# Kernel tuning notes

Measured on AMD Instinct MI355X. Metric: run time of the kernel, lower is better.

## Reference

```python
import jax, jax.numpy as jnp
import numpy as np
from jax import lax

N = 4096
INPUT_SIZE = 2048
HIDDEN = 256
HEADS = 4
T_POWER = 6
K_KNN = 30   # N >= 300 branch in compute_markov_tensor_optic
KA = 10      # int(k/3)


def setup_inputs() -> dict:
    key = jax.random.key(0)
    k1, k2, k3, k4, k5 = jax.random.split(key, 5)
    bound = 1.0 / np.sqrt(INPUT_SIZE)
    return {
        "input_tensor": jax.random.normal(k1, (N, INPUT_SIZE), dtype=jnp.float32),
        "Wq": jax.random.uniform(k2, (HEADS, HIDDEN, INPUT_SIZE), jnp.float32, -bound, bound),
        "bq": jax.random.uniform(k3, (HEADS, HIDDEN), jnp.float32, -bound, bound),
        "Wk": jax.random.uniform(k4, (HEADS, HIDDEN, INPUT_SIZE), jnp.float32, -bound, bound),
        "bk": jax.random.uniform(k5, (HEADS, HIDDEN), jnp.float32, -bound, bound),
    }


def _markov(q, k):
    # q, k: [N, HIDDEN]; pairwise Euclidean distances via gram trick
    sq = (jnp.sum(q * q, axis=1)[:, None]
          + jnp.sum(k * k, axis=1)[None, :]
          - 2.0 * (q @ k.T))
    d = jnp.sqrt(jnp.maximum(sq, 0.0) + 1e-10)          # [N, N]
    # adaptive bandwidth: (KA)-th smallest distance per row
    md = jnp.sort(d, axis=1)[:, KA]                      # [N]
    d = d / (md[:, None] + 1e-10)
    aff = jnp.exp(-(d ** 2))                             # epsilon = 1
    # knn pruning: keep entries >= k-th largest per row
    kth = lax.top_k(aff, K_KNN)[0][:, -1]                # [N]
    aff = aff * (aff >= kth[:, None]).astype(aff.dtype)
    idx = jnp.arange(aff.shape[0])
    aff = aff.at[idx, idx].set(1.0)
    return aff + aff.T


def reference(input_tensor, Wq, bq, Wk, bk):
    # per-head projections: [HEADS, N, HIDDEN]
    q = jnp.einsum('nd,hkd->hnk', input_tensor, Wq) + bq[:, None, :]
    k = jnp.einsum('nd,hkd->hnk', input_tensor, Wk) + bk[:, None, :]
    aff = jax.vmap(_markov)(q, k)                        # [HEADS, N, N]
    probs = jax.nn.softmax(aff, axis=-1)
    probs_t = jnp.linalg.matrix_power(probs, T_POWER)    # batched matrix power
    ctx = jnp.einsum('hnm,md->hnd', probs_t, input_tensor)  # [HEADS, N, INPUT_SIZE]
    return jnp.mean(ctx, axis=0)
```

## Files before the change

### kernel.cpp

```cpp
#include <hip/hip_runtime.h>
#include <hip/hip_bf16.h>
#include <math.h>

#define NN 4096
#define DIN 2048
#define HID 256
#define NHEADS 4
#define CAP 1024
#define OVF_CAP 131072
#define PW 128

__global__ __launch_bounds__(256) void proj_kernel(
    const float* __restrict__ X, const float* __restrict__ Wq, const float* __restrict__ bq,
    const float* __restrict__ Wk, const float* __restrict__ bk,
    float* __restrict__ qbuf, float* __restrict__ kbuf, int h)
{
    const int isK = blockIdx.z;
    const float* W    = (isK ? Wk : Wq) + (size_t)h * HID * DIN;
    const float* bias = (isK ? bk : bq) + h * HID;
    float* out = isK ? kbuf : qbuf;

    const int bm = blockIdx.x * 64;
    const int bn = blockIdx.y * 64;
    const int t  = threadIdx.x;
    const int tx = t & 15, ty = t >> 4;
    const int lr = t >> 2, lk = (t & 3) * 4;

    __shared__ float As[16][68];
    __shared__ float Bs[16][68];
    float acc[4][4] = {};

    for (int k0 = 0; k0 < DIN; k0 += 16) {
        float4 av = *(const float4*)(X + (size_t)(bm + lr) * DIN + k0 + lk);
        float4 bv = *(const float4*)(W + (size_t)(bn + lr) * DIN + k0 + lk);
        As[lk+0][lr]=av.x; As[lk+1][lr]=av.y; As[lk+2][lr]=av.z; As[lk+3][lr]=av.w;
        Bs[lk+0][lr]=bv.x; Bs[lk+1][lr]=bv.y; Bs[lk+2][lr]=bv.z; Bs[lk+3][lr]=bv.w;
        __syncthreads();
        #pragma unroll
        for (int kk = 0; kk < 16; ++kk) {
            const float4 a4 = *(const float4*)&As[kk][ty*4];
            const float4 b4 = *(const float4*)&Bs[kk][tx*4];
            const float a[4] = {a4.x,a4.y,a4.z,a4.w};
            const float b[4] = {b4.x,b4.y,b4.z,b4.w};
            #pragma unroll
            for (int i = 0; i < 4; ++i)
                #pragma unroll
                for (int j = 0; j < 4; ++j)
                    acc[i][j] = fmaf(a[i], b[j], acc[i][j]);
        }
        __syncthreads();
    }
    #pragma unroll
    for (int i = 0; i < 4; ++i) {
        const int m = bm + ty*4 + i;
        float4 o;
        o.x = acc[i][0] + bias[bn+tx*4+0];
        o.y = acc[i][1] + bias[bn+tx*4+1];
        o.z = acc[i][2] + bias[bn+tx*4+2];
        o.w = acc[i][3] + bias[bn+tx*4+3];
        *(float4*)(out + (size_t)m * HID + bn + tx*4) = o;
    }
}

__global__ __launch_bounds__(64) void rownorm_kernel(
    const float* __restrict__ q, const float* __restrict__ k,
    float* __restrict__ sqq, float* __restrict__ sqk)
{
    const int row = blockIdx.x;
    const int lane = threadIdx.x;
    const float* src = (blockIdx.y ? k : q) + (size_t)row * HID;
    float4 v = *(const float4*)(src + lane * 4);
    float s = v.x*v.x + v.y*v.y + v.z*v.z + v.w*v.w;
    for (int off = 32; off; off >>= 1) s += __shfl_down(s, off);
    if (lane == 0) (blockIdx.y ? sqk : sqq)[row] = s;
}

__global__ __launch_bounds__(256) void dist_kernel(
    const float* __restrict__ q, const float* __restrict__ k,
    const float* __restrict__ sqq, const float* __restrict__ sqk,
    float* __restrict__ Dm)
{
    const int bm = blockIdx.x * 64;
    const int bn = blockIdx.y * 64;
    const int t  = threadIdx.x;
    const int tx = t & 15, ty = t >> 4;
    const int lr = t >> 2, lk = (t & 3) * 4;

    __shared__ float As[16][68];
    __shared__ float Bs[16][68];
    float acc[4][4] = {};

    for (int k0 = 0; k0 < HID; k0 += 16) {
        float4 av = *(const float4*)(q + (size_t)(bm + lr) * HID + k0 + lk);
        float4 bv = *(const float4*)(k + (size_t)(bn + lr) * HID + k0 + lk);
        As[lk+0][lr]=av.x; As[lk+1][lr]=av.y; As[lk+2][lr]=av.z; As[lk+3][lr]=av.w;
        Bs[lk+0][lr]=bv.x; Bs[lk+1][lr]=bv.y; Bs[lk+2][lr]=bv.z; Bs[lk+3][lr]=bv.w;
        __syncthreads();
        #pragma unroll
        for (int kk = 0; kk < 16; ++kk) {
            const float4 a4 = *(const float4*)&As[kk][ty*4];
            const float4 b4 = *(const float4*)&Bs[kk][tx*4];
            const float a[4] = {a4.x,a4.y,a4.z,a4.w};
            const float b[4] = {b4.x,b4.y,b4.z,b4.w};
            #pragma unroll
            for (int i = 0; i < 4; ++i)
                #pragma unroll
                for (int j = 0; j < 4; ++j)
                    acc[i][j] = fmaf(a[i], b[j], acc[i][j]);
        }
        __syncthreads();
    }
    #pragma unroll
    for (int i = 0; i < 4; ++i) {
        const int m = bm + ty*4 + i;
        const float sm = sqq[m];
        float4 o;
        float v0 = sm + sqk[bn+tx*4+0] - 2.0f*acc[i][0];
        float v1 = sm + sqk[bn+tx*4+1] - 2.0f*acc[i][1];
        float v2 = sm + sqk[bn+tx*4+2] - 2.0f*acc[i][2];
        float v3 = sm + sqk[bn+tx*4+3] - 2.0f*acc[i][3];
        o.x = sqrtf(fmaxf(v0, 0.0f) + 1e-10f);
        o.y = sqrtf(fmaxf(v1, 0.0f) + 1e-10f);
        o.z = sqrtf(fmaxf(v2, 0.0f) + 1e-10f);
        o.w = sqrtf(fmaxf(v3, 0.0f) + 1e-10f);
        *(float4*)(Dm + (size_t)m * NN + bn + tx*4) = o;
    }
}

__device__ unsigned radix_kth_smallest(const unsigned* s, int lane, int K)
{
    unsigned lo = 0u, hi = 0xFFFFFFFFu;
    while (lo < hi) {
        unsigned mid = lo + ((hi - lo) >> 1);
        int c = 0;
        #pragma unroll 8
        for (int i = 0; i < 64; ++i) c += (s[i*64 + lane] <= mid) ? 1 : 0;
        for (int off = 32; off; off >>= 1) c += __shfl_xor(c, off);
        if (c >= K) hi = mid; else lo = mid + 1;
    }
    return lo;
}

__global__ __launch_bounds__(64) void select_kernel(
    const float* __restrict__ Dm, float* __restrict__ mdp, float* __restrict__ kth)
{
    __shared__ unsigned s[NN];
    const int row = blockIdx.x;
    const int lane = threadIdx.x;
    const float* src = Dm + (size_t)row * NN;
    for (int c = 0; c < 16; ++c) {
        const int base = c*256 + lane*4;
        float4 v = *(const float4*)(src + base);
        s[base+0] = __float_as_uint(v.x);
        s[base+1] = __float_as_uint(v.y);
        s[base+2] = __float_as_uint(v.z);
        s[base+3] = __float_as_uint(v.w);
    }
    __syncthreads();
    unsigned v11 = radix_kth_smallest(s, lane, 11);
    unsigned v30 = radix_kth_smallest(s, lane, 30);
    if (lane == 0) {
        float md = __uint_as_float(v11) + 1e-10f;
        float t  = __uint_as_float(v30) / md;
        mdp[row] = md;
        kth[row] = expf(-(t*t));
    }
}

__global__ __launch_bounds__(256) void aff_kernel(
    float* __restrict__ Dm, const float* __restrict__ mdp, const float* __restrict__ kthv)
{
    const size_t idx4 = ((size_t)blockIdx.x * 256 + threadIdx.x) * 4;
    const int i = (int)(idx4 >> 12);
    const int j = (int)(idx4 & 4095);
    const float m = mdp[i];
    const float kt = kthv[i];
    float4 v = *(float4*)(Dm + idx4);
    float t0 = v.x / m, t1 = v.y / m, t2 = v.z / m, t3 = v.w / m;
    float a0 = expf(-(t0*t0)), a1 = expf(-(t1*t1)), a2 = expf(-(t2*t2)), a3 = expf(-(t3*t3));
    a0 = (a0 >= kt) ? a0 : 0.0f;
    a1 = (a1 >= kt) ? a1 : 0.0f;
    a2 = (a2 >= kt) ? a2 : 0.0f;
    a3 = (a3 >= kt) ? a3 : 0.0f;
    if (j+0 == i) a0 = 1.0f;
    if (j+1 == i) a1 = 1.0f;
    if (j+2 == i) a2 = 1.0f;
    if (j+3 == i) a3 = 1.0f;
    v.x = a0; v.y = a1; v.z = a2; v.w = a3;
    *(float4*)(Dm + idx4) = v;
}

__global__ __launch_bounds__(256) void sym_kernel(float* __restrict__ Dm)
{
    int rem = blockIdx.x;
    int bi = 0;
    while (rem >= 64 - bi) { rem -= 64 - bi; ++bi; }
    const int bj = bi + rem;

    __shared__ float T1[64][65];
    __shared__ float T2[64][65];
    const int t = threadIdx.x;
    const int lr = t >> 4;
    const int lc4 = (t & 15) * 4;

    #pragma unroll
    for (int rr = 0; rr < 4; ++rr) {
        const int r = rr*16 + lr;
        float4 v1 = *(const float4*)(Dm + (size_t)(bi*64 + r) * NN + bj*64 + lc4);
        T1[r][lc4+0]=v1.x; T1[r][lc4+1]=v1.y; T1[r][lc4+2]=v1.z; T1[r][lc4+3]=v1.w;
        float4 v2 = *(const float4*)(Dm + (size_t)(bj*64 + r) * NN + bi*64 + lc4);
        T2[r][lc4+0]=v2.x; T2[r][lc4+1]=v2.y; T2[r][lc4+2]=v2.z; T2[r][lc4+3]=v2.w;
    }
    __syncthreads();
    #pragma unroll
    for (int rr = 0; rr < 4; ++rr) {
        const int r = rr*16 + lr;
        float4 o1;
        o1.x = T1[r][lc4+0] + T2[lc4+0][r];
        o1.y = T1[r][lc4+1] + T2[lc4+1][r];
        o1.z = T1[r][lc4+2] + T2[lc4+2][r];
        o1.w = T1[r][lc4+3] + T2[lc4+3][r];
        *(float4*)(Dm + (size_t)(bi*64 + r) * NN + bj*64 + lc4) = o1;
        if (bi != bj) {
            float4 o2;
            o2.x = T2[r][lc4+0] + T1[lc4+0][r];
            o2.y = T2[r][lc4+1] + T1[lc4+1][r];
            o2.z = T2[r][lc4+2] + T1[lc4+2][r];
            o2.w = T2[r][lc4+3] + T1[lc4+3][r];
            *(float4*)(Dm + (size_t)(bj*64 + r) * NN + bi*64 + lc4) = o2;
        }
    }
}

__global__ __launch_bounds__(64) void zero_ovf_kernel(int* __restrict__ ovf_cnt)
{
    if (threadIdx.x == 0) *ovf_cnt = 0;
}

__global__ __launch_bounds__(256) void stats_extract_kernel(
    const float* __restrict__ A, float* __restrict__ cvec, int* __restrict__ nnz,
    int* __restrict__ cols, float* __restrict__ vals,
    int* __restrict__ ovf_cnt, int* __restrict__ ovf_row,
    int* __restrict__ ovf_col, float* __restrict__ ovf_val)
{
    __shared__ float srow[NN];
    __shared__ float red[8];
    __shared__ int cnt;
    const int row = blockIdx.x, t = threadIdx.x;
    const int lane = t & 63, wid = t >> 6;
    const float* src = A + (size_t)row * NN;

    float mx = -1e30f;
    #pragma unroll
    for (int c = 0; c < 4; ++c) {
        const int base = c*1024 + t*4;
        float4 v = *(const float4*)(src + base);
        *(float4*)&srow[base] = v;
        mx = fmaxf(mx, fmaxf(fmaxf(v.x, v.y), fmaxf(v.z, v.w)));
    }
    for (int off = 32; off; off >>= 1) mx = fmaxf(mx, __shfl_xor(mx, off));
    if (lane == 0) red[wid] = mx;
    __syncthreads();
    mx = fmaxf(fmaxf(red[0], red[1]), fmaxf(red[2], red[3]));

    float sum = 0.0f;
    #pragma unroll
    for (int c = 0; c < 4; ++c) {
        const int base = c*1024 + t*4;
        float4 v = *(float4*)&srow[base];
        sum += expf(v.x-mx) + expf(v.y-mx) + expf(v.z-mx) + expf(v.w-mx);
    }
    for (int off = 32; off; off >>= 1) sum += __shfl_xor(sum, off);
    if (lane == 0) red[4 + wid] = sum;
    if (t == 0) cnt = 0;
    __syncthreads();
    sum = red[4] + red[5] + red[6] + red[7];
    const float ci = expf(-mx) / sum;
    if (t == 0) cvec[row] = ci;

    for (int c = 0; c < 16; ++c) {
        const int j = c*256 + t;
        const float a = srow[j];
        if (a != 0.0f) {
            const float v = expf(a - mx)/sum - ci;
            int p = atomicAdd(&cnt, 1);
            if (p < CAP) {
                cols[(size_t)row*CAP + p] = j;
                vals[(size_t)row*CAP + p] = v;
            } else {
                int q = atomicAdd(ovf_cnt, 1);
                if (q < OVF_CAP) {
                    ovf_row[q] = row;
                    ovf_col[q] = j;
                    ovf_val[q] = v;
                }
            }
        }
    }
    __syncthreads();
    if (t == 0) {
        const int c2 = min(cnt, CAP);
        const int e2 = min((c2 + 7) & ~7, CAP);
        for (int p = c2; p < e2; ++p) {
            cols[(size_t)row*CAP + p] = 0;
            vals[(size_t)row*CAP + p] = 0.0f;
        }
        nnz[row] = e2 == c2 ? c2 : e2;
    }
}

__global__ __launch_bounds__(256) void colsum_partial_kernel(
    const float* __restrict__ Y, float* __restrict__ part)
{
    const int cc = blockIdx.y * 256 + threadIdx.x;
    const int r0 = blockIdx.x * 128;
    float s = 0.0f;
    for (int r = 0; r < 128; ++r) s += Y[(size_t)(r0 + r) * DIN + cc];
    part[(size_t)blockIdx.x * DIN + cc] = s;
}

__global__ __launch_bounds__(256) void colsum_final_kernel(
    const float* __restrict__ part, float* __restrict__ colsum)
{
    const int cc = blockIdx.x * 256 + threadIdx.x;
    float s = 0.0f;
    #pragma unroll
    for (int r = 0; r < 32; ++r) s += part[(size_t)r * DIN + cc];
    colsum[cc] = s;
}

__global__ __launch_bounds__(256) void spmm_kernel(
    const float* __restrict__ Y, const float* __restrict__ colsum,
    const float* __restrict__ cvec, const int* __restrict__ nnz,
    const int* __restrict__ cols, const float* __restrict__ vals,
    float* __restrict__ Yout, int mode)
{
    const int wave = threadIdx.x >> 6, lane = threadIdx.x & 63;
    const int row = __builtin_amdgcn_readfirstlane(blockIdx.x * 4 + wave);
    const int c = blockIdx.y * PW + lane * 2;

    const int n = nnz[row];
    const float ci = cvec[row];
    const int*   rc = cols + (size_t)row * CAP;
    const float* rv = vals + (size_t)row * CAP;

    const float2 s = *(const float2*)(colsum + c);
    float ax = ci * s.x, ay = ci * s.y;

    for (int base = 0; base < n; base += 8) {
        float2 y[8];
        #pragma unroll
        for (int u = 0; u < 8; ++u) {
            const int j = rc[base + u];
            y[u] = *(const float2*)(Y + (size_t)j * DIN + c);
        }
        #pragma unroll
        for (int u = 0; u < 8; ++u) {
            const float v = rv[base + u];
            ax = fmaf(v, y[u].x, ax);
            ay = fmaf(v, y[u].y, ay);
        }
    }

    float* dst = Yout + (size_t)row * DIN + c;
    float2 o;
    if (mode == 0)      { o.x = ax;       o.y = ay; }
    else if (mode == 1) { o.x = 0.25f*ax; o.y = 0.25f*ay; }
    else {
        const float2 p = *(const float2*)dst;
        o.x = p.x + 0.25f*ax; o.y = p.y + 0.25f*ay;
    }
    *(float2*)dst = o;
}

__global__ __launch_bounds__(256) void spmm_fixup_kernel(
    const float* __restrict__ Y, const int* __restrict__ ovf_cnt,
    const int* __restrict__ ovf_row, const int* __restrict__ ovf_col,
    const float* __restrict__ ovf_val, float* __restrict__ Yout, float scale)
{
    const int cnt = min(*ovf_cnt, OVF_CAP);
    const int t = threadIdx.x;
    for (int e = blockIdx.x; e < cnt; e += gridDim.x) {
        const int i = ovf_row[e], j = ovf_col[e];
        const float v = ovf_val[e] * scale;
        const float* yr = Y + (size_t)j * DIN;
        float* dst = Yout + (size_t)i * DIN;
        #pragma unroll
        for (int c = t*4; c < DIN; c += 1024) {
            atomicAdd(dst + c + 0, v * yr[c + 0]);
            atomicAdd(dst + c + 1, v * yr[c + 1]);
            atomicAdd(dst + c + 2, v * yr[c + 2]);
            atomicAdd(dst + c + 3, v * yr[c + 3]);
        }
    }
}

extern "C" void kernel_launch(void* const* d_in, const int* in_sizes, int n_in,
                              void* d_out, int out_size, void* d_ws, size_t ws_size,
                              hipStream_t stream)
{
    const float* X  = (const float*)d_in[0];
    const float* Wq = (const float*)d_in[1];
    const float* bq = (const float*)d_in[2];
    const float* Wk = (const float*)d_in[3];
    const float* bk = (const float*)d_in[4];
    float* out = (float*)d_out;

    float* ws   = (float*)d_ws;
    float* qbuf = ws;
    float* kbuf = qbuf + (size_t)NN*HID;
    float* A    = kbuf + (size_t)NN*HID;
    float* Y1   = A;
    float* Y2   = A + (size_t)NN*DIN;
    float* valsA= A + (size_t)NN*NN;
    int*   colsA= (int*)(valsA + (size_t)NN*CAP);
    float* part = (float*)(colsA + (size_t)NN*CAP);
    float* colsum = part + 32*DIN;
    float* sqq  = colsum + DIN;
    float* sqk  = sqq + NN;
    float* mdp  = sqk + NN;
    float* kth  = mdp + NN;
    float* cvec = kth + NN;
    int*   nnz  = (int*)(cvec + NN);
    int*   ovf_cnt = nnz + NN;
    int*   ovf_row = ovf_cnt + 16;
    int*   ovf_col = ovf_row + OVF_CAP;
    float* ovf_val = (float*)(ovf_col + OVF_CAP);

    for (int h = 0; h < NHEADS; ++h) {
        proj_kernel<<<dim3(NN/64, HID/64, 2), 256, 0, stream>>>(X, Wq, bq, Wk, bk, qbuf, kbuf, h);
        rownorm_kernel<<<dim3(NN, 2), 64, 0, stream>>>(qbuf, kbuf, sqq, sqk);
        dist_kernel<<<dim3(NN/64, NN/64), 256, 0, stream>>>(qbuf, kbuf, sqq, sqk, A);
        select_kernel<<<dim3(NN), 64, 0, stream>>>(A, mdp, kth);
        aff_kernel<<<dim3(NN*NN/1024), 256, 0, stream>>>(A, mdp, kth);
        sym_kernel<<<dim3(2080), 256, 0, stream>>>(A);
        zero_ovf_kernel<<<dim3(1), 64, 0, stream>>>(ovf_cnt);
        stats_extract_kernel<<<dim3(NN), 256, 0, stream>>>(A, cvec, nnz, colsA, valsA,
                                                           ovf_cnt, ovf_row, ovf_col, ovf_val);

        const float* src = X;
        for (int tpow = 1; tpow <= 6; ++tpow) {
            colsum_partial_kernel<<<dim3(32, DIN/256), 256, 0, stream>>>(src, part);
            colsum_final_kernel<<<dim3(DIN/256), 256, 0, stream>>>(part, colsum);
            float* dst;
            int mode;
            if (tpow == 6)      { dst = out; mode = (h == 0) ? 1 : 2; }
            else if (tpow & 1)  { dst = Y1;  mode = 0; }
            else                { dst = Y2;  mode = 0; }
            spmm_kernel<<<dim3(NN/4, DIN/PW), 256, 0, stream>>>(src, colsum, cvec, nnz, colsA, valsA, dst, mode);
            spmm_fixup_kernel<<<dim3(64), 256, 0, stream>>>(src, ovf_cnt, ovf_row, ovf_col, ovf_val,
                                                            dst, (tpow == 6) ? 0.25f : 1.0f);
            src = dst;
        }
    }
}
```

Measured before the change: 7.247 ms.

## Remap SpMM grid to XCD-local column panels and double-buffer gathers

The SpMM grid is flattened to 1D and each block index is decoded so that every XCD (id&7) works on a fixed column panel across row blocks. The aim is to keep the gathered Y columns resident in that XCD's L2 instead of spreading them across all dies. The gather loop becomes a software-pipelined double buffer, so the next 8 row loads are issued while FMAs run on the previous 8. Output stores now use nontemporal hints. The tradeoffs are higher register pressure from the two buffers and a dependence on the hardware's round-robin block-to-XCD dispatch.

```diff
diff --git a/kernel.cpp b/kernel.cpp
--- a/kernel.cpp
+++ b/kernel.cpp
@@ -329,6 +329,23 @@
     colsum[cc] = s;
 }
 
+typedef float vf2 __attribute__((ext_vector_type(2)));
+
+#define SPMM_LOAD(buf, b)                                               \
+    _Pragma("unroll")                                                   \
+    for (int u = 0; u < 8; ++u) {                                       \
+        const int j = rc[(b) + u];                                      \
+        buf[u] = *(const float2*)(Y + (size_t)j * DIN + c);             \
+    }
+
+#define SPMM_FMA(buf, b)                                                \
+    _Pragma("unroll")                                                   \
+    for (int u = 0; u < 8; ++u) {                                       \
+        const float v = rv[(b) + u];                                    \
+        ax = fmaf(v, buf[u].x, ax);                                     \
+        ay = fmaf(v, buf[u].y, ay);                                     \
+    }
+
 __global__ __launch_bounds__(256) void spmm_kernel(
     const float* __restrict__ Y, const float* __restrict__ colsum,
     const float* __restrict__ cvec, const int* __restrict__ nnz,
@@ -336,8 +353,15 @@
     float* __restrict__ Yout, int mode)
 {
     const int wave = threadIdx.x >> 6, lane = threadIdx.x & 63;
-    const int row = __builtin_amdgcn_readfirstlane(blockIdx.x * 4 + wave);
-    const int c = blockIdx.y * PW + lane * 2;
+
+    const int id     = blockIdx.x;
+    const int xcd    = id & 7;
+    const int w      = id >> 3;
+    const int panel  = xcd + ((w & 1024) ? 8 : 0);
+    const int rowblk = w & 1023;
+
+    const int row = __builtin_amdgcn_readfirstlane(rowblk * 4 + wave);
+    const int c = panel * PW + lane * 2;
 
     const int n = nnz[row];
     const float ci = cvec[row];
@@ -347,30 +371,35 @@
     const float2 s = *(const float2*)(colsum + c);
     float ax = ci * s.x, ay = ci * s.y;
 
-    for (int base = 0; base < n; base += 8) {
-        float2 y[8];
-        #pragma unroll
-        for (int u = 0; u < 8; ++u) {
-            const int j = rc[base + u];
-            y[u] = *(const float2*)(Y + (size_t)j * DIN + c);
-        }
-        #pragma unroll
-        for (int u = 0; u < 8; ++u) {
-            const float v = rv[base + u];
-            ax = fmaf(v, y[u].x, ax);
-            ay = fmaf(v, y[u].y, ay);
-        }
-    }
+    float2 yA[8], yB[8];
+    SPMM_LOAD(yA, 0);
+    int base = 8;
+    bool tailA = true;
+    while (base < n) {
+        SPMM_LOAD(yB, base);
+        SPMM_FMA(yA, base - 8);
+        base += 8;
+        if (base < n) {
+            SPMM_LOAD(yA, base);
+            SPMM_FMA(yB, base - 8);
+            base += 8;
+        } else {
+            SPMM_FMA(yB, base - 8);
+            tailA = false;
+            break;
+        }
+    }
+    if (tailA) { SPMM_FMA(yA, base - 8); }
 
     float* dst = Yout + (size_t)row * DIN + c;
-    float2 o;
-    if (mode == 0)      { o.x = ax;       o.y = ay; }
-    else if (mode == 1) { o.x = 0.25f*ax; o.y = 0.25f*ay; }
+    vf2 o;
+    if (mode == 0)      { o[0] = ax;       o[1] = ay; }
+    else if (mode == 1) { o[0] = 0.25f*ax; o[1] = 0.25f*ay; }
     else {
-        const float2 p = *(const float2*)dst;
-        o.x = p.x + 0.25f*ax; o.y = p.y + 0.25f*ay;
-    }
-    *(float2*)dst = o;
+        const vf2 p = __builtin_nontemporal_load((const vf2*)dst);
+        o[0] = p[0] + 0.25f*ax; o[1] = p[1] + 0.25f*ay;
+    }
+    __builtin_nontemporal_store(o, (vf2*)dst);
 }
 
 __global__ __launch_bounds__(256) void spmm_fixup_kernel(
@@ -447,7 +476,7 @@
             if (tpow == 6)      { dst = out; mode = (h == 0) ? 1 : 2; }
             else if (tpow & 1)  { dst = Y1;  mode = 0; }
             else                { dst = Y2;  mode = 0; }
-            spmm_kernel<<<dim3(NN/4, DIN/PW), 256, 0, stream>>>(src, colsum, cvec, nnz, colsA, valsA, dst, mode);
+            spmm_kernel<<<dim3((NN/4) * (DIN/PW)), 256, 0, stream>>>(src, colsum, cvec, nnz, colsA, valsA, dst, mode);
             spmm_fixup_kernel<<<dim3(64), 256, 0, stream>>>(src, ovf_cnt, ovf_row, ovf_col, ovf_val,
                                                             dst, (tpow == 6) ? 0.25f : 1.0f);
             src = dst;
```

Measured after the change: 6.648 ms. 1.09x faster.
